# Kernel optimization log

Measured on AMD Instinct MI355X. Metric: run time of the kernel, lower is better.

Reference implementation:

```python
import jax, jax.numpy as jnp
import numpy as np
import math

B, S, D, H = 2, 2048, 1024, 16
DH = D // H


def setup_inputs() -> dict:
    key = jax.random.key(0)
    ks = jax.random.split(key, 10)
    scale = 1.0 / math.sqrt(D)
    inp = {
        "x": jax.random.normal(ks[0], (B, S, D), dtype=jnp.float32),
        "valid_nums": jax.random.randint(ks[1], (B,), 1, S + 1, dtype=jnp.int32),
        "Wq": jax.random.normal(ks[2], (D, D), dtype=jnp.float32) * scale,
        "bq": jnp.zeros((D,), dtype=jnp.float32),
        "Wk": jax.random.normal(ks[3], (D, D), dtype=jnp.float32) * scale,
        "bk": jnp.zeros((D,), dtype=jnp.float32),
        "Wv": jax.random.normal(ks[4], (D, D), dtype=jnp.float32) * scale,
        "bv": jnp.zeros((D,), dtype=jnp.float32),
        "Wo": jax.random.normal(ks[5], (D, D), dtype=jnp.float32) * scale,
        "bo": jnp.zeros((D,), dtype=jnp.float32),
    }
    return inp


def _split_heads(t):
    # (B, S, D) -> (B, H, S, DH)
    return t.reshape(B, S, H, DH).transpose(0, 2, 1, 3)


def reference(x, valid_nums, Wq, bq, Wk, bk, Wv, bv, Wo, bo):
    q = _split_heads(x @ Wq + bq)
    k = _split_heads(x @ Wk + bk)
    v = _split_heads(x @ Wv + bv)
    scores = jnp.einsum("bhqd,bhkd->bhqk", q, k) / math.sqrt(DH)  # (B,H,S,S)
    # length mask over keys: key j valid iff j < valid_nums[b]
    key_mask = jnp.arange(S)[None, :] < valid_nums[:, None]        # (B,S)
    scores = jnp.where(key_mask[:, None, None, :], scores, -jnp.inf)
    attn = jax.nn.softmax(scores, axis=-1)
    out = jnp.einsum("bhqk,bhkd->bhqd", attn, v)                   # (B,H,S,DH)
    out = out.transpose(0, 2, 1, 3).reshape(B, S, D)
    return out @ Wo + bo
```

## Files before the change

### kernel.cpp

```cpp
#include <hip/hip_runtime.h>
#include <hip/hip_bf16.h>
#include <math.h>

static constexpr int Bb = 2, Ss = 2048, Dd = 1024, Hh = 16, DHh = 64;
static constexpr int Mm = Bb * Ss;
static constexpr int Kk = Dd;

typedef __attribute__((ext_vector_type(8))) short bf16x8;
typedef __attribute__((ext_vector_type(4))) float f32x4;
typedef unsigned short us;

__device__ inline short f2b(float f) {
    __hip_bfloat16 h = __float2bfloat16(f);
    return *reinterpret_cast<short*>(&h);
}
__device__ inline float b2f(us u) {
    __hip_bfloat16 h = *reinterpret_cast<__hip_bfloat16*>(&u);
    return __bfloat162float(h);
}
__device__ inline unsigned pk2(float lo, float hi) {
    return ((unsigned)(us)f2b(hi) << 16) | (unsigned)(us)f2b(lo);
}
__device__ inline float ex2(float x) {
    return __builtin_amdgcn_exp2f(x);
}

__device__ inline void gload16(us* lds, const us* g) {
    __builtin_amdgcn_global_load_lds(
        (const __attribute__((address_space(1))) void*)g,
        (__attribute__((address_space(3))) void*)lds,
        16, 0, 0);
}

__global__ __launch_bounds__(256)
void prep_kernel(const float* __restrict__ x, us* __restrict__ xb,
                 const float* __restrict__ Wq, const float* __restrict__ Wk,
                 const float* __restrict__ Wv, const float* __restrict__ Wo,
                 us* __restrict__ Wt, us* __restrict__ Woth, us* __restrict__ Wotl)
{
    __shared__ float T[64][65];
    const int id = blockIdx.x;
    const int tid = threadIdx.x;

    if (id < 2048) {
        const size_t i = ((size_t)id * 256 + tid) * 8;
        float4 a = *(const float4*)(x + i);
        float4 b = *(const float4*)(x + i + 4);
        bf16x8 t;
        t[0] = f2b(a.x); t[1] = f2b(a.y); t[2] = f2b(a.z); t[3] = f2b(a.w);
        t[4] = f2b(b.x); t[5] = f2b(b.y); t[6] = f2b(b.z); t[7] = f2b(b.w);
        *(bf16x8*)(xb + i) = t;
        return;
    }

    const int w = id - 2048;
    const int z = w >> 8;
    const int rem = w & 255;
    const int n0 = (rem & 15) * 64, k0 = (rem >> 4) * 64;
    const float* W = (z == 0) ? Wq : (z == 1) ? Wk : (z == 2) ? Wv : Wo;
    const int split = (z == 3);
    us* dh = split ? Woth : (Wt + (size_t)z * Dd * Kk);
    us* dl = Wotl;

    const int r = tid >> 2, c0 = (tid & 3) * 16;
#pragma unroll
    for (int j = 0; j < 4; ++j) {
        float4 v = *(const float4*)(W + (size_t)(k0 + r) * Dd + n0 + c0 + 4 * j);
        T[r][c0 + 4 * j + 0] = v.x;
        T[r][c0 + 4 * j + 1] = v.y;
        T[r][c0 + 4 * j + 2] = v.z;
        T[r][c0 + 4 * j + 3] = v.w;
    }
    __syncthreads();
    us hi[16], lo[16];
#pragma unroll
    for (int j = 0; j < 16; ++j) {
        float v = T[c0 + j][r];
        us h = (us)f2b(v);
        hi[j] = h;
        if (split) lo[j] = (us)f2b(v - b2f(h));
    }
    *(bf16x8*)&dh[(size_t)(n0 + r) * Kk + k0 + c0]     = *(bf16x8*)&hi[0];
    *(bf16x8*)&dh[(size_t)(n0 + r) * Kk + k0 + c0 + 8] = *(bf16x8*)&hi[8];
    if (split) {
        *(bf16x8*)&dl[(size_t)(n0 + r) * Kk + k0 + c0]     = *(bf16x8*)&lo[0];
        *(bf16x8*)&dl[(size_t)(n0 + r) * Kk + k0 + c0 + 8] = *(bf16x8*)&lo[8];
    }
}

__global__ __launch_bounds__(512)
void gemm_qkv_kernel(const us* __restrict__ xb, const us* __restrict__ Wt,
                     const float* __restrict__ bq, const float* __restrict__ bk,
                     const float* __restrict__ bv, us* __restrict__ QKV)
{
    __shared__ us As[128 * 64];
    __shared__ us Bs[128 * 64];
    const int tid = threadIdx.x;
    const int wave = tid >> 6, lane = tid & 63;
    const int wr = wave >> 2, wc = wave & 3;
    const int lg = lane >> 4, ll = lane & 15;

    const int id = blockIdx.x;
    const int col0 = (id >> 5) * 128;
    const int row0 = (id & 31) * 128;

    f32x4 acc[4][2];
#pragma unroll
    for (int mt = 0; mt < 4; ++mt)
#pragma unroll
        for (int nt = 0; nt < 2; ++nt)
#pragma unroll
            for (int r = 0; r < 4; ++r) acc[mt][nt][r] = 0.f;

    const int srow = tid >> 3;
    const int scol = (tid & 7) * 8;
    const us* Ag = xb + (size_t)(row0 + srow) * Kk + scol;
    const us* Bg = Wt + (size_t)(col0 + srow) * Kk + scol;
    us* Ad = &As[(wave * 8) * 64];
    us* Bd = &Bs[(wave * 8) * 64];

    for (int k0 = 0; k0 < Kk; k0 += 64) {
        __syncthreads();
#pragma unroll
        for (int i = 0; i < 2; ++i) {
            gload16(Ad + (i * 64) * 64, Ag + (size_t)(i * 64) * Kk + k0);
            gload16(Bd + (i * 64) * 64, Bg + (size_t)(i * 64) * Kk + k0);
        }
        __syncthreads();
#pragma unroll
        for (int ks = 0; ks < 2; ++ks) {
            bf16x8 af[4], bfr[2];
#pragma unroll
            for (int mt = 0; mt < 4; ++mt)
                af[mt] = *(const bf16x8*)&As[(wr * 64 + mt * 16 + ll) * 64 + ks * 32 + lg * 8];
#pragma unroll
            for (int nt = 0; nt < 2; ++nt)
                bfr[nt] = *(const bf16x8*)&Bs[(wc * 32 + nt * 16 + ll) * 64 + ks * 32 + lg * 8];
#pragma unroll
            for (int mt = 0; mt < 4; ++mt)
#pragma unroll
                for (int nt = 0; nt < 2; ++nt)
                    acc[mt][nt] = __builtin_amdgcn_mfma_f32_16x16x32_bf16(af[mt], bfr[nt], acc[mt][nt], 0, 0, 0);
        }
    }

    const int z = col0 >> 10;
    const int c0 = col0 & 1023;
    const float* bias = (z == 0) ? bq : (z == 1) ? bk : bv;
    const float osc = (z == 0) ? 0.125f * 1.44269504f : 1.0f;
    us* outz = QKV + (size_t)z * Mm * Dd;

    if (z == 2) {
#pragma unroll
        for (int mt = 0; mt < 4; ++mt)
#pragma unroll
            for (int nt = 0; nt < 2; ++nt) {
                int row = row0 + wr * 64 + mt * 16 + lg * 4;
                int col = c0 + wc * 32 + nt * 16 + ll;
                int b_ = row >> 11, s_ = row & 2047;
                float bv_ = bias[col];
                union { us u[4]; uint2 d2; } pk;
#pragma unroll
                for (int r = 0; r < 4; ++r) pk.u[r] = (us)f2b(acc[mt][nt][r] + bv_);
                *(uint2*)&outz[((size_t)(b_ * Hh * DHh) + col) * Ss + s_] = pk.d2;
            }
    } else {
#pragma unroll
        for (int mt = 0; mt < 4; ++mt)
#pragma unroll
            for (int nt = 0; nt < 2; ++nt)
#pragma unroll
                for (int r = 0; r < 4; ++r) {
                    int row = row0 + wr * 64 + mt * 16 + lg * 4 + r;
                    int col = c0 + wc * 32 + nt * 16 + ll;
                    float v = (acc[mt][nt][r] + bias[col]) * osc;
                    int b_ = row >> 11, s_ = row & 2047, h_ = col >> 6, d_ = col & 63;
                    outz[(((size_t)(b_ * Hh + h_)) * Ss + s_) * DHh + d_] = (us)f2b(v);
                }
    }
}

__global__ __launch_bounds__(256)
void gemm_final_kernel(const us* __restrict__ Oh, const us* __restrict__ Ol,
                       const us* __restrict__ Wth, const us* __restrict__ Wtl,
                       const float* __restrict__ bo, float* __restrict__ out)
{
    __shared__ us AhS[128 * 64];
    __shared__ us AlS[128 * 64];
    __shared__ us BhS[64 * 64];
    __shared__ us BlS[64 * 64];
    const int tid = threadIdx.x;
    const int wave = tid >> 6, lane = tid & 63;
    const int wr = wave >> 1, wc = wave & 1;
    const int lg = lane >> 4, ll = lane & 15;

    const int id = blockIdx.x;
    const int col0 = (id >> 5) * 64;
    const int row0 = (id & 31) * 128;

    f32x4 acc[4][2];
#pragma unroll
    for (int mt = 0; mt < 4; ++mt)
#pragma unroll
        for (int nt = 0; nt < 2; ++nt)
#pragma unroll
            for (int r = 0; r < 4; ++r) acc[mt][nt][r] = 0.f;

    const size_t aoff = (size_t)(row0 + wave * 32 + (lane >> 3)) * Kk + (lane & 7) * 8;
    const size_t boff = (size_t)(col0 + wave * 16 + (lane >> 3)) * Kk + (lane & 7) * 8;
    const us* Ahg = Oh + aoff;
    const us* Alg = Ol + aoff;
    const us* Bhg = Wth + boff;
    const us* Blg = Wtl + boff;
    us* AhD = &AhS[(wave * 4) * 512];
    us* AlD = &AlS[(wave * 4) * 512];
    us* BhD = &BhS[(wave * 2) * 512];
    us* BlD = &BlS[(wave * 2) * 512];

    for (int k0 = 0; k0 < Kk; k0 += 64) {
        __syncthreads();
#pragma unroll
        for (int i = 0; i < 4; ++i) {
            gload16(AhD + i * 512, Ahg + (size_t)(i * 8) * Kk + k0);
            gload16(AlD + i * 512, Alg + (size_t)(i * 8) * Kk + k0);
        }
#pragma unroll
        for (int j2 = 0; j2 < 2; ++j2) {
            gload16(BhD + j2 * 512, Bhg + (size_t)(j2 * 8) * Kk + k0);
            gload16(BlD + j2 * 512, Blg + (size_t)(j2 * 8) * Kk + k0);
        }
        __syncthreads();
#pragma unroll
        for (int ks = 0; ks < 2; ++ks) {
            bf16x8 ah[4], al[4], bh[2], bl[2];
#pragma unroll
            for (int mt = 0; mt < 4; ++mt) {
                ah[mt] = *(const bf16x8*)&AhS[(wr * 64 + mt * 16 + ll) * 64 + ks * 32 + lg * 8];
                al[mt] = *(const bf16x8*)&AlS[(wr * 64 + mt * 16 + ll) * 64 + ks * 32 + lg * 8];
            }
#pragma unroll
            for (int nt = 0; nt < 2; ++nt) {
                bh[nt] = *(const bf16x8*)&BhS[(wc * 32 + nt * 16 + ll) * 64 + ks * 32 + lg * 8];
                bl[nt] = *(const bf16x8*)&BlS[(wc * 32 + nt * 16 + ll) * 64 + ks * 32 + lg * 8];
            }
#pragma unroll
            for (int mt = 0; mt < 4; ++mt)
#pragma unroll
                for (int nt = 0; nt < 2; ++nt) {
                    acc[mt][nt] = __builtin_amdgcn_mfma_f32_16x16x32_bf16(ah[mt], bh[nt], acc[mt][nt], 0, 0, 0);
                    acc[mt][nt] = __builtin_amdgcn_mfma_f32_16x16x32_bf16(al[mt], bh[nt], acc[mt][nt], 0, 0, 0);
                    acc[mt][nt] = __builtin_amdgcn_mfma_f32_16x16x32_bf16(ah[mt], bl[nt], acc[mt][nt], 0, 0, 0);
                }
        }
    }

#pragma unroll
    for (int mt = 0; mt < 4; ++mt)
#pragma unroll
        for (int nt = 0; nt < 2; ++nt)
#pragma unroll
            for (int r = 0; r < 4; ++r) {
                int row = row0 + wr * 64 + mt * 16 + lg * 4 + r;
                int col = col0 + wc * 32 + nt * 16 + ll;
                out[(size_t)row * Dd + col] = acc[mt][nt][r] + bo[col];
            }
}

__global__ __launch_bounds__(512)
void attn_mfma_kernel(const us* __restrict__ Q, const us* __restrict__ K,
                      const us* __restrict__ Vt_g, const int* __restrict__ valid_nums,
                      us* __restrict__ Oh, us* __restrict__ Ol)
{
    const int id  = blockIdx.x;
    const int bh  = id >> 4;
    const int qb  = id & 15;
    const int b   = bh >> 4, h = bh & 15;
    const int q0  = qb * 128;

    const int tid  = threadIdx.x;
    const int wave = tid >> 6;
    const int lane = tid & 63;
    const int lg = lane >> 4;
    const int ll = lane & 15;

    const int nv = valid_nums[b];
    const int ntiles = (nv + 127) >> 7;

    const us* Qb = Q    + (size_t)bh * Ss * DHh;
    const us* Kb = K    + (size_t)bh * Ss * DHh;
    const us* Vb = Vt_g + (size_t)bh * DHh * Ss;

    __shared__ us Ks[128][72];
    __shared__ us Vs[64][136];

    bf16x8 qa[2];
    {
        const us* qrow = Qb + (size_t)(q0 + wave * 16 + ll) * DHh;
        qa[0] = *(const bf16x8*)(qrow + lg * 8);
        qa[1] = *(const bf16x8*)(qrow + 32 + lg * 8);
    }

    union { unsigned w[4]; bf16x8 v; } ones_u;
#pragma unroll
    for (int i = 0; i < 4; ++i) ones_u.w[i] = 0x3F803F80u;
    const bf16x8 vones = ones_u.v;

    f32x4 o[4], o4;
#pragma unroll
    for (int nt = 0; nt < 4; ++nt) { o[nt][0]=0.f; o[nt][1]=0.f; o[nt][2]=0.f; o[nt][3]=0.f; }
    o4[0]=0.f; o4[1]=0.f; o4[2]=0.f; o4[3]=0.f;
    float mq = -INFINITY;

    const int krow = tid >> 3;
    const int scol = (tid & 7) * 8;

    bf16x8 kr0 = *(const bf16x8*)(Kb + (size_t)krow * DHh + scol);
    bf16x8 kr1 = *(const bf16x8*)(Kb + (size_t)(64 + krow) * DHh + scol);
    bf16x8 vr0 = *(const bf16x8*)(Vb + (size_t)krow * Ss + scol);
    bf16x8 vr1 = *(const bf16x8*)(Vb + (size_t)krow * Ss + 64 + scol);

    const int l0 = (2 * (lg & 1)) * 16 + ll;
    const int l1 = l0 + 16;
    const bool hi = (lg & 2);

    for (int kt = 0; kt < ntiles; ++kt) {
        const int k0 = kt << 7;
        __syncthreads();
        *(bf16x8*)&Ks[krow][scol]      = kr0;
        *(bf16x8*)&Ks[krow + 64][scol] = kr1;
        *(bf16x8*)&Vs[krow][scol]      = vr0;
        *(bf16x8*)&Vs[krow][64 + scol] = vr1;
        __syncthreads();
        if (kt + 1 < ntiles) {
            const int kn = k0 + 128;
            kr0 = *(const bf16x8*)(Kb + (size_t)(kn + krow) * DHh + scol);
            kr1 = *(const bf16x8*)(Kb + (size_t)(kn + 64 + krow) * DHh + scol);
            vr0 = *(const bf16x8*)(Vb + (size_t)krow * Ss + kn + scol);
            vr1 = *(const bf16x8*)(Vb + (size_t)krow * Ss + kn + 64 + scol);
        }

        f32x4 s[8];
#pragma unroll
        for (int nt = 0; nt < 8; ++nt) { s[nt][0]=0.f; s[nt][1]=0.f; s[nt][2]=0.f; s[nt][3]=0.f; }
        __builtin_amdgcn_s_setprio(1);
#pragma unroll
        for (int ks = 0; ks < 2; ++ks) {
#pragma unroll
            for (int nt = 0; nt < 8; ++nt) {
                bf16x8 kf = *(const bf16x8*)&Ks[nt * 16 + ll][ks * 32 + lg * 8];
                s[nt] = __builtin_amdgcn_mfma_f32_16x16x32_bf16(kf, qa[ks], s[nt], 0, 0, 0);
            }
        }
        __builtin_amdgcn_s_setprio(0);

        float mx;
        if (k0 + 128 <= nv) {
            mx = -INFINITY;
#pragma unroll
            for (int nt = 0; nt < 8; ++nt)
#pragma unroll
                for (int r = 0; r < 4; ++r) mx = fmaxf(mx, s[nt][r]);
        } else {
            mx = -INFINITY;
#pragma unroll
            for (int nt = 0; nt < 8; ++nt)
#pragma unroll
                for (int r = 0; r < 4; ++r) {
                    int key = k0 + nt * 16 + lg * 4 + r;
                    float v = (key < nv) ? s[nt][r] : -INFINITY;
                    s[nt][r] = v;
                    mx = fmaxf(mx, v);
                }
        }
        mx = fmaxf(mx, __shfl_xor(mx, 16));
        mx = fmaxf(mx, __shfl_xor(mx, 32));

        const bool rescale = !__all(mx <= mq + 11.5f);
        if (rescale) {
            float mn = fmaxf(mq, mx);
            float corr = ex2(mq - mn);
            mq = mn;
            float corr4[4];
#pragma unroll
            for (int r = 0; r < 4; ++r) corr4[r] = __shfl(corr, lg * 16 + lg * 4 + r);
#pragma unroll
            for (int nt = 0; nt < 4; ++nt)
#pragma unroll
                for (int r = 0; r < 4; ++r) o[nt][r] *= corr4[r];
#pragma unroll
            for (int r = 0; r < 4; ++r) o4[r] *= corr4[r];
        }

#pragma unroll
        for (int g = 0; g < 4; ++g) {
            float pA[4], pB[4];
#pragma unroll
            for (int r = 0; r < 4; ++r) {
                pA[r] = ex2(s[2 * g][r] - mq);
                pB[r] = ex2(s[2 * g + 1][r] - mq);
            }
            unsigned dA0 = pk2(pA[0], pA[1]), dA1 = pk2(pA[2], pA[3]);
            unsigned dB0 = pk2(pB[0], pB[1]), dB1 = pk2(pB[2], pB[3]);

            unsigned a0 = (unsigned)__shfl((int)dA0, l0);
            unsigned a1 = (unsigned)__shfl((int)dA1, l0);
            unsigned a2 = (unsigned)__shfl((int)dA0, l1);
            unsigned a3 = (unsigned)__shfl((int)dA1, l1);
            unsigned b0 = (unsigned)__shfl((int)dB0, l0);
            unsigned b1 = (unsigned)__shfl((int)dB1, l0);
            unsigned b2 = (unsigned)__shfl((int)dB0, l1);
            unsigned b3 = (unsigned)__shfl((int)dB1, l1);
            union { unsigned w[4]; bf16x8 v; } pa;
            pa.w[0] = hi ? b0 : a0;
            pa.w[1] = hi ? b1 : a1;
            pa.w[2] = hi ? b2 : a2;
            pa.w[3] = hi ? b3 : a3;

            __builtin_amdgcn_s_setprio(1);
#pragma unroll
            for (int nt = 0; nt < 4; ++nt) {
                bf16x8 vb = *(const bf16x8*)&Vs[nt * 16 + ll][g * 32 + lg * 8];
                o[nt] = __builtin_amdgcn_mfma_f32_16x16x32_bf16(pa.v, vb, o[nt], 0, 0, 0);
            }
            o4 = __builtin_amdgcn_mfma_f32_16x16x32_bf16(pa.v, vones, o4, 0, 0, 0);
            __builtin_amdgcn_s_setprio(0);
        }
    }

#pragma unroll
    for (int r = 0; r < 4; ++r) {
        int row = q0 + wave * 16 + lg * 4 + r;
        float linv = 1.f / o4[r];
#pragma unroll
        for (int nt = 0; nt < 4; ++nt) {
            float val = o[nt][r] * linv;
            us uh = (us)f2b(val);
            float rem = val - b2f(uh);
            size_t base = ((size_t)b * Ss + row) * Dd + h * DHh + nt * 16 + ll;
            Oh[base] = uh;
            Ol[base] = (us)f2b(rem);
        }
    }
}

extern "C" void kernel_launch(void* const* d_in, const int* in_sizes, int n_in,
                              void* d_out, int out_size, void* d_ws, size_t ws_size,
                              hipStream_t stream) {
    const float* x     = (const float*)d_in[0];
    const int*   valid = (const int*)d_in[1];
    const float* Wq = (const float*)d_in[2];
    const float* bq = (const float*)d_in[3];
    const float* Wk = (const float*)d_in[4];
    const float* bk = (const float*)d_in[5];
    const float* Wv = (const float*)d_in[6];
    const float* bv = (const float*)d_in[7];
    const float* Wo = (const float*)d_in[8];
    const float* bo = (const float*)d_in[9];

    const size_t per = (size_t)Mm * Dd;
    const size_t wsz = (size_t)Dd * Kk;
    us* wsp  = (us*)d_ws;
    us* QKV  = wsp;
    us* Wt   = QKV + 3 * per;
    us* OhB  = Wt + 3 * wsz;
    us* OlB  = OhB + per;
    us* Woth = OlB + per;
    us* Wotl = Woth + wsz;
    us* xb   = Wotl + wsz;

    prep_kernel<<<2048 + 1024, 256, 0, stream>>>(
        x, xb, Wq, Wk, Wv, Wo, Wt, Woth, Wotl);

    gemm_qkv_kernel<<<768, 512, 0, stream>>>(xb, Wt, bq, bk, bv, QKV);

    attn_mfma_kernel<<<(Ss / 128) * (Bb * Hh), 512, 0, stream>>>(
        QKV, QKV + per, QKV + 2 * per, valid, OhB, OlB);

    gemm_final_kernel<<<512, 256, 0, stream>>>(
        OhB, OlB, Woth, Wotl, bo, (float*)d_out);
}
```

Measured before the change: 136.1 us.

## Double-buffer K/V tiles in shared memory for attention loop

Turns the single K/V LDS buffer into a ping-pong pair. The next tile is written to LDS while the current one is computed, and global loads are issued two tiles ahead. This drops one __syncthreads per iteration and overlaps the LDS stores with the QK MFMA work. In exchange it doubles LDS use per block, which may lower occupancy.

```diff
diff --git a/kernel.cpp b/kernel.cpp
--- a/kernel.cpp
+++ b/kernel.cpp
@@ -290,8 +290,8 @@
     const us* Kb = K    + (size_t)bh * Ss * DHh;
     const us* Vb = Vt_g + (size_t)bh * DHh * Ss;
 
-    __shared__ us Ks[128][72];
-    __shared__ us Vs[64][136];
+    __shared__ us Ks[2][128][72];
+    __shared__ us Vs[2][64][136];
 
     bf16x8 qa[2];
     {
@@ -314,44 +314,58 @@
     const int krow = tid >> 3;
     const int scol = (tid & 7) * 8;
 
+    const int l0 = (2 * (lg & 1)) * 16 + ll;
+    const int l1 = l0 + 16;
+    const bool hi = (lg & 2);
+
     bf16x8 kr0 = *(const bf16x8*)(Kb + (size_t)krow * DHh + scol);
     bf16x8 kr1 = *(const bf16x8*)(Kb + (size_t)(64 + krow) * DHh + scol);
     bf16x8 vr0 = *(const bf16x8*)(Vb + (size_t)krow * Ss + scol);
     bf16x8 vr1 = *(const bf16x8*)(Vb + (size_t)krow * Ss + 64 + scol);
-
-    const int l0 = (2 * (lg & 1)) * 16 + ll;
-    const int l1 = l0 + 16;
-    const bool hi = (lg & 2);
+    *(bf16x8*)&Ks[0][krow][scol]      = kr0;
+    *(bf16x8*)&Ks[0][krow + 64][scol] = kr1;
+    *(bf16x8*)&Vs[0][krow][scol]      = vr0;
+    *(bf16x8*)&Vs[0][krow][64 + scol] = vr1;
+    if (1 < ntiles) {
+        kr0 = *(const bf16x8*)(Kb + (size_t)(128 + krow) * DHh + scol);
+        kr1 = *(const bf16x8*)(Kb + (size_t)(128 + 64 + krow) * DHh + scol);
+        vr0 = *(const bf16x8*)(Vb + (size_t)krow * Ss + 128 + scol);
+        vr1 = *(const bf16x8*)(Vb + (size_t)krow * Ss + 128 + 64 + scol);
+    }
 
     for (int kt = 0; kt < ntiles; ++kt) {
+        const int p = kt & 1;
         const int k0 = kt << 7;
         __syncthreads();
-        *(bf16x8*)&Ks[krow][scol]      = kr0;
-        *(bf16x8*)&Ks[krow + 64][scol] = kr1;
-        *(bf16x8*)&Vs[krow][scol]      = vr0;
-        *(bf16x8*)&Vs[krow][64 + scol] = vr1;
-        __syncthreads();
+
+
+        f32x4 s[8];
+#pragma unroll
+        for (int nt = 0; nt < 8; ++nt) { s[nt][0]=0.f; s[nt][1]=0.f; s[nt][2]=0.f; s[nt][3]=0.f; }
+        __builtin_amdgcn_s_setprio(1);
+#pragma unroll
+        for (int ks = 0; ks < 2; ++ks) {
+#pragma unroll
+            for (int nt = 0; nt < 8; ++nt) {
+                bf16x8 kf = *(const bf16x8*)&Ks[p][nt * 16 + ll][ks * 32 + lg * 8];
+                s[nt] = __builtin_amdgcn_mfma_f32_16x16x32_bf16(kf, qa[ks], s[nt], 0, 0, 0);
+            }
+        }
+        __builtin_amdgcn_s_setprio(0);
+
         if (kt + 1 < ntiles) {
-            const int kn = k0 + 128;
+            *(bf16x8*)&Ks[p ^ 1][krow][scol]      = kr0;
+            *(bf16x8*)&Ks[p ^ 1][krow + 64][scol] = kr1;
+            *(bf16x8*)&Vs[p ^ 1][krow][scol]      = vr0;
+            *(bf16x8*)&Vs[p ^ 1][krow][64 + scol] = vr1;
+        }
+        if (kt + 2 < ntiles) {
+            const int kn = k0 + 256;
             kr0 = *(const bf16x8*)(Kb + (size_t)(kn + krow) * DHh + scol);
             kr1 = *(const bf16x8*)(Kb + (size_t)(kn + 64 + krow) * DHh + scol);
             vr0 = *(const bf16x8*)(Vb + (size_t)krow * Ss + kn + scol);
             vr1 = *(const bf16x8*)(Vb + (size_t)krow * Ss + kn + 64 + scol);
         }
-
-        f32x4 s[8];
-#pragma unroll
-        for (int nt = 0; nt < 8; ++nt) { s[nt][0]=0.f; s[nt][1]=0.f; s[nt][2]=0.f; s[nt][3]=0.f; }
-        __builtin_amdgcn_s_setprio(1);
-#pragma unroll
-        for (int ks = 0; ks < 2; ++ks) {
-#pragma unroll
-            for (int nt = 0; nt < 8; ++nt) {
-                bf16x8 kf = *(const bf16x8*)&Ks[nt * 16 + ll][ks * 32 + lg * 8];
-                s[nt] = __builtin_amdgcn_mfma_f32_16x16x32_bf16(kf, qa[ks], s[nt], 0, 0, 0);
-            }
-        }
-        __builtin_amdgcn_s_setprio(0);
 
         float mx;
         if (k0 + 128 <= nv) {
@@ -419,7 +433,7 @@
             __builtin_amdgcn_s_setprio(1);
 #pragma unroll
             for (int nt = 0; nt < 4; ++nt) {
-                bf16x8 vb = *(const bf16x8*)&Vs[nt * 16 + ll][g * 32 + lg * 8];
+                bf16x8 vb = *(const bf16x8*)&Vs[p][nt * 16 + ll][g * 32 + lg * 8];
                 o[nt] = __builtin_amdgcn_mfma_f32_16x16x32_bf16(pa.v, vb, o[nt], 0, 0, 0);
             }
             o4 = __builtin_amdgcn_mfma_f32_16x16x32_bf16(pa.v, vones, o4, 0, 0, 0);
```

Result: no change. 136.4 us (+0.2%).
